# Kernel tuning notes

Measured on AMD Instinct MI355X. Metric: run time of the kernel, lower is better.

The kernel has to match this reference:

```python
import jax, jax.numpy as jnp
import numpy as np

L = 3          # num_layers
H = 128        # hidden_dim
NH = 4         # num heads
DH = H // NH   # head dim
B = 32         # graphs per batch
N = 1024       # nodes per graph
NTOT = B * N
DEG = 16
E = NTOT * DEG
BN_EPS = 1e-5


def setup_inputs() -> dict:
    key = jax.random.key(0)
    ks = jax.random.split(key, 16)
    s = 1.0 / np.sqrt(H)
    inp = {
        "x": jax.random.normal(ks[0], (NTOT, H), jnp.float32),
        "edge_attr": jax.random.normal(ks[1], (E, H), jnp.float32),
        "gine_w1": jax.random.normal(ks[2], (L, H, H), jnp.float32) * s,
        "gine_b1": jnp.zeros((L, H), jnp.float32),
        "gine_bn_g": jnp.ones((L, H), jnp.float32),
        "gine_bn_b": jnp.zeros((L, H), jnp.float32),
        "gine_w2": jax.random.normal(ks[3], (L, H, H), jnp.float32) * s,
        "gine_b2": jnp.zeros((L, H), jnp.float32),
        "attn_wqkv": jax.random.normal(ks[4], (L, 3 * H, H), jnp.float32) * s,
        "attn_bqkv": jnp.zeros((L, 3 * H), jnp.float32),
        "attn_wo": jax.random.normal(ks[5], (L, H, H), jnp.float32) * s,
        "attn_bo": jnp.zeros((L, H), jnp.float32),
        "norm1_g": jnp.ones((L, H), jnp.float32),
        "norm1_b": jnp.zeros((L, H), jnp.float32),
        "norm2_g": jnp.ones((L, H), jnp.float32),
        "norm2_b": jnp.zeros((L, H), jnp.float32),
        "norm3_g": jnp.ones((L, H), jnp.float32),
        "norm3_b": jnp.zeros((L, H), jnp.float32),
        "mlp_w1": jax.random.normal(ks[6], (L, 2 * H, H), jnp.float32) * s,
        "mlp_b1": jnp.zeros((L, 2 * H), jnp.float32),
        "mlp_w2": jax.random.normal(ks[7], (L, H, 2 * H), jnp.float32) * (1.0 / np.sqrt(2 * H)),
        "mlp_b2": jnp.zeros((L, H), jnp.float32),
    }
    # intra-graph random edges: local src/dst in [0, N) plus per-graph offset
    offs = (jnp.arange(E, dtype=jnp.int32) // (N * DEG)) * N  # graph offset per edge
    src = jax.random.randint(ks[8], (E,), 0, N, jnp.int32) + offs
    dst = jax.random.randint(ks[9], (E,), 0, N, jnp.int32) + offs
    inp["edge_index"] = jnp.stack([src, dst]).astype(jnp.int32)
    inp["batch"] = (jnp.arange(NTOT, dtype=jnp.int32) // N)
    return inp


def _bn(x, g, b):
    m = x.mean(axis=0)
    v = jnp.var(x, axis=0)
    return (x - m) * jax.lax.rsqrt(v + BN_EPS) * g + b


def _gps_forward(x, edge_attr, gine_w1, gine_b1, gine_bn_g, gine_bn_b, gine_w2, gine_b2,
                 attn_wqkv, attn_bqkv, attn_wo, attn_bo,
                 norm1_g, norm1_b, norm2_g, norm2_b, norm3_g, norm3_b,
                 mlp_w1, mlp_b1, mlp_w2, mlp_b2, edge_index, batch):
    src, dst = edge_index[0], edge_index[1]
    for i in range(L):
        # ---- GINEConv: msg = relu(x_j + e), sum-scatter, nn-MLP on x + aggr (eps=0)
        msg = jax.nn.relu(x[src] + edge_attr)                       # [E, H]
        aggr = jax.ops.segment_sum(msg, dst, num_segments=NTOT)     # [NTOT, H]
        h = x + aggr
        h = h @ gine_w1[i].T + gine_b1[i]
        h = jax.nn.relu(_bn(h, gine_bn_g[i], gine_bn_b[i]))
        h = h @ gine_w2[i].T + gine_b2[i]
        h_local = _bn(h + x, norm1_g[i], norm1_b[i])                # residual + norm1
        # ---- global multi-head attention on x (dense per-graph, equal sizes)
        xb = x.reshape(B, N, H)
        qkv = xb @ attn_wqkv[i].T + attn_bqkv[i]                    # [B, N, 3H]
        q, k, v = jnp.split(qkv, 3, axis=-1)
        q = q.reshape(B, N, NH, DH).transpose(0, 2, 1, 3)           # [B, nh, N, dh]
        k = k.reshape(B, N, NH, DH).transpose(0, 2, 1, 3)
        v = v.reshape(B, N, NH, DH).transpose(0, 2, 1, 3)
        scores = jnp.einsum("bhqd,bhkd->bhqk", q, k) / np.sqrt(DH)
        attn = jax.nn.softmax(scores, axis=-1)
        o = jnp.einsum("bhqk,bhkd->bhqd", attn, v)
        o = o.transpose(0, 2, 1, 3).reshape(B, N, H) @ attn_wo[i].T + attn_bo[i]
        h_attn = _bn(o.reshape(NTOT, H) + x, norm2_g[i], norm2_b[i])
        # ---- combine + FFN + norm3
        out = h_local + h_attn
        ff = jax.nn.relu(out @ mlp_w1[i].T + mlp_b1[i]) @ mlp_w2[i].T + mlp_b2[i]
        x = _bn(out + ff, norm3_g[i], norm3_b[i])
        if i != L - 1:
            x = jax.nn.relu(x)
    return x


def reference(x, edge_attr, gine_w1, gine_b1, gine_bn_g, gine_bn_b, gine_w2, gine_b2,
              attn_wqkv, attn_bqkv, attn_wo, attn_bo,
              norm1_g, norm1_b, norm2_g, norm2_b, norm3_g, norm3_b,
              mlp_w1, mlp_b1, mlp_w2, mlp_b2, edge_index, batch):
    return _gps_forward(x, edge_attr, gine_w1, gine_b1, gine_bn_g, gine_bn_b, gine_w2, gine_b2,
                        attn_wqkv, attn_bqkv, attn_wo, attn_bo,
                        norm1_g, norm1_b, norm2_g, norm2_b, norm3_g, norm3_b,
                        mlp_w1, mlp_b1, mlp_w2, mlp_b2, edge_index, batch)
```

## Files before the change

kernel.cpp:

```cpp
#include <hip/hip_runtime.h>
#include <hip/hip_bf16.h>
#include <math.h>

#define NTOT 32768
#define HDIM 128
#define NE   524288
#define NGRAPH 32
#define NNODE 1024
#define NHEAD 4
#define DHEAD 32

typedef __attribute__((ext_vector_type(8))) short bf8v;
typedef __attribute__((ext_vector_type(4))) float f4v;
typedef unsigned short u16;

__device__ __forceinline__ float4 ld4(const float* p){ return *(const float4*)p; }

__device__ __forceinline__ u16 bf16rn(float f){
  union { float f; unsigned u; } x; x.f = f;
  unsigned r = x.u + 0x7FFF + ((x.u >> 16) & 1);
  return (u16)(r >> 16);
}
__device__ __forceinline__ unsigned pk2(float a, float b){
  unsigned r;
  asm("v_cvt_pk_bf16_f32 %0, %1, %2" : "=v"(r) : "v"(a), "v"(b));
  return r;
}
__device__ __forceinline__ float bf2f(u16 u){
  union { unsigned u; float f; } x; x.u = ((unsigned)u) << 16;
  return x.f;
}

__global__ void k_count(const int* __restrict__ dst, int* __restrict__ deg){
  int e = blockIdx.x*256 + threadIdx.x;
  atomicAdd(&deg[dst[e]], 1);
}

__global__ __launch_bounds__(1024) void k_scan(const int* __restrict__ deg,
                                               int* __restrict__ indptr,
                                               int* __restrict__ cursor){
  __shared__ int sm[1024];
  int t = threadIdx.x;
  int base = t*32;
  int s = 0;
  for (int j=0;j<32;j++) s += deg[base+j];
  sm[t] = s; __syncthreads();
  for (int off=1; off<1024; off<<=1){
    int v = (t>=off) ? sm[t-off] : 0;
    __syncthreads();
    sm[t] += v;
    __syncthreads();
  }
  int ex = sm[t] - s;
  for (int j=0;j<32;j++){
    int d = deg[base+j];
    indptr[base+j] = ex; cursor[base+j] = ex;
    ex += d;
  }
  if (t == 1023) indptr[NTOT] = ex;
}

__global__ void k_fill(const int* __restrict__ dst, int* __restrict__ cursor,
                       int* __restrict__ perm){
  int e = blockIdx.x*256 + threadIdx.x;
  int pos = atomicAdd(&cursor[dst[e]], 1);
  perm[pos] = e;
}

__global__ __launch_bounds__(256) void k_eaprep(const float* __restrict__ ea,
    const int* __restrict__ src, const int* __restrict__ perm,
    u16* __restrict__ EAb, int* __restrict__ SRCp){
  int tid = threadIdx.x;
  int p = blockIdx.x*8 + (tid>>5);
  int c4 = (tid&31)*4;
  int e = perm[p];
  float4 v = ld4(&ea[(size_t)e*HDIM + c4]);
  uint2 o; o.x = pk2(v.x, v.y); o.y = pk2(v.z, v.w);
  *(uint2*)&EAb[(size_t)p*HDIM + c4] = o;
  if ((tid&31) == 0) SRCp[p] = src[e];
}

__global__ __launch_bounds__(256) void k_xprep(const float* __restrict__ x, u16* __restrict__ Xb){
  size_t i = ((size_t)blockIdx.x*256 + threadIdx.x)*4;
  float4 v = ld4(&x[i]);
  uint2 o; o.x = pk2(v.x,v.y); o.y = pk2(v.z,v.w);
  *(uint2*)&Xb[i] = o;
}

__global__ __launch_bounds__(256) void k_wprep(const float* s0,const float* s1,const float* s2,
    const float* s3,const float* s4,const float* s5, u16* __restrict__ Wb){
  const float* srcs[6] = {s0,s1,s2,s3,s4,s5};
  const int cnt4[6] = {12288,12288,36864,12288,24576,24576};
  const int off[6]  = {0,49152,98304,245760,294912,393216};
  int y = blockIdx.y;
  int i = blockIdx.x*256 + threadIdx.x;
  if (i >= cnt4[y]) return;
  float4 v = ld4(&srcs[y][(size_t)i*4]);
  uint2 o; o.x = pk2(v.x,v.y); o.y = pk2(v.z,v.w);
  *(uint2*)&Wb[off[y] + (size_t)i*4] = o;
}

__global__ __launch_bounds__(256) void k_aggr(const u16* __restrict__ Xb,
                       const u16* __restrict__ EAb,
                       const int* __restrict__ SRCp, const int* __restrict__ indptr,
                       u16* __restrict__ Hb){
  int tid = threadIdx.x;
  int n = blockIdx.x*8 + (tid>>5);
  int c4 = (tid&31)*4;
  int p0 = indptr[n], p1 = indptr[n+1];
  float a0=0.f,a1=0.f,a2=0.f,a3=0.f;
  for (int p=p0;p<p1;p++){
    int s = SRCp[p];
    uint2 xv = *(const uint2*)&Xb[(size_t)s*HDIM + c4];
    uint2 ev = *(const uint2*)&EAb[(size_t)p*HDIM + c4];
    a0 += fmaxf(bf2f((u16)(xv.x&0xffff)) + bf2f((u16)(ev.x&0xffff)), 0.f);
    a1 += fmaxf(bf2f((u16)(xv.x>>16))    + bf2f((u16)(ev.x>>16)), 0.f);
    a2 += fmaxf(bf2f((u16)(xv.y&0xffff)) + bf2f((u16)(ev.y&0xffff)), 0.f);
    a3 += fmaxf(bf2f((u16)(xv.y>>16))    + bf2f((u16)(ev.y>>16)), 0.f);
  }
  uint2 xn = *(const uint2*)&Xb[(size_t)n*HDIM + c4];
  a0 += bf2f((u16)(xn.x&0xffff)); a1 += bf2f((u16)(xn.x>>16));
  a2 += bf2f((u16)(xn.y&0xffff)); a3 += bf2f((u16)(xn.y>>16));
  uint2 o; o.x = pk2(a0,a1); o.y = pk2(a2,a3);
  *(uint2*)&Hb[(size_t)n*HDIM + c4] = o;
}

template<bool BNA, bool DUAL, bool RELU, bool EP, bool STATS, bool WROUT>
__global__ __launch_bounds__(256) void k_bgemm(const u16* __restrict__ Ab,
    const u16* __restrict__ A2b,
    const float* __restrict__ slotA, const float* __restrict__ gA, const float* __restrict__ bA,
    const float* __restrict__ slotB, const float* __restrict__ gB, const float* __restrict__ bB,
    const u16* __restrict__ Wb, const float* __restrict__ bias,
    const u16* __restrict__ Epb, u16* __restrict__ Cb,
    u16* __restrict__ OUTb, float* __restrict__ slotOut, int N, int K){
  __shared__ float sbnA[256];
  __shared__ float sbnB[256];
  __shared__ float sred[128];
  int tid = threadIdx.x;
  int w = tid>>6, l = tid&63;
  int q = l&15, g = l>>4;
  int m0 = blockIdx.x*128, n0 = blockIdx.y*64;
  int wr = w*32;
  const float invn = 1.0f/32768.0f;
  if (BNA || DUAL){
    if (tid < 128){
      float mean = slotA[tid]*invn;
      float var  = slotA[128+tid]*invn - mean*mean;
      float sc = gA[tid] * rsqrtf(var + 1e-5f);
      sbnA[tid] = sc; sbnA[128+tid] = bA[tid] - mean*sc;
      if (DUAL){
        float mean2 = slotB[tid]*invn;
        float var2  = slotB[128+tid]*invn - mean2*mean2;
        float sc2 = gB[tid] * rsqrtf(var2 + 1e-5f);
        sbnB[tid] = sc2; sbnB[128+tid] = bB[tid] - mean2*sc2;
      }
    }
  }
  if (STATS && tid < 128) sred[tid] = 0.f;
  if (BNA || DUAL || STATS) __syncthreads();

  f4v acc[2][4];
  #pragma unroll
  for (int i=0;i<2;i++)
    #pragma unroll
    for (int j=0;j<4;j++) acc[i][j] = (f4v){0.f,0.f,0.f,0.f};

  for (int kc=0; kc<K; kc+=32){
    bf8v af[2], bfv[4];
    #pragma unroll
    for (int mt=0;mt<2;mt++){
      int row = m0 + wr + 16*mt + q;
      if (!BNA && !DUAL){
        af[mt] = *(const bf8v*)&Ab[(size_t)row*K + kc + 8*g];
      } else {
        union { bf8v b; u16 s[8]; unsigned u[4]; } ra, r2, ro;
        ra.b = *(const bf8v*)&Ab[(size_t)row*K + kc + 8*g];
        if (DUAL) r2.b = *(const bf8v*)&A2b[(size_t)row*K + kc + 8*g];
        float v[8];
        #pragma unroll
        for (int j=0;j<8;j++){
          int kk = kc + 8*g + j;
          float f = bf2f(ra.s[j]) * sbnA[kk] + sbnA[128+kk];
          if (BNA) f = fmaxf(f, 0.f);
          if (DUAL) f += bf2f(r2.s[j]) * sbnB[kk] + sbnB[128+kk];
          v[j] = f;
        }
        ro.u[0]=pk2(v[0],v[1]); ro.u[1]=pk2(v[2],v[3]);
        ro.u[2]=pk2(v[4],v[5]); ro.u[3]=pk2(v[6],v[7]);
        af[mt] = ro.b;
        if (WROUT && blockIdx.y == 0)
          *(uint4*)&OUTb[(size_t)row*K + kc + 8*g] = *(uint4*)ro.u;
      }
    }
    #pragma unroll
    for (int nt=0;nt<4;nt++){
      int col = n0 + 16*nt + q;
      bfv[nt] = *(const bf8v*)&Wb[(size_t)col*K + kc + 8*g];
    }
    #pragma unroll
    for (int mt=0;mt<2;mt++)
      #pragma unroll
      for (int nt=0;nt<4;nt++)
        acc[mt][nt] = __builtin_amdgcn_mfma_f32_16x16x32_bf16(af[mt], bfv[nt], acc[mt][nt], 0,0,0);
  }
  float bbv[4];
  #pragma unroll
  for (int nt=0;nt<4;nt++) bbv[nt] = bias[n0 + 16*nt + q];
  float csum[4] = {0.f,0.f,0.f,0.f}, csq[4] = {0.f,0.f,0.f,0.f};
  #pragma unroll
  for (int mt=0;mt<2;mt++){
    int row0 = m0 + wr + 16*mt + 4*g;
    #pragma unroll
    for (int nt=0;nt<4;nt++){
      int col = n0 + 16*nt + q;
      #pragma unroll
      for (int r=0;r<4;r++){
        size_t off = (size_t)(row0+r)*N + col;
        float v = acc[mt][nt][r] + bbv[nt];
        if (EP) v += bf2f(Epb[off]);
        if (RELU) v = fmaxf(v, 0.f);
        Cb[off] = bf16rn(v);
        if (STATS){ csum[nt] += v; csq[nt] += v*v; }
      }
    }
  }
  if (STATS){
    #pragma unroll
    for (int nt=0;nt<4;nt++){
      int c = 16*nt + q;
      atomicAdd(&sred[c], csum[nt]);
      atomicAdd(&sred[64+c], csq[nt]);
    }
    __syncthreads();
    if (tid < 64){
      atomicAdd(&slotOut[n0+tid], sred[tid]);
      atomicAdd(&slotOut[128+n0+tid], sred[64+tid]);
    }
  }
}

__global__ __launch_bounds__(256) void k_qkvgemm(const u16* __restrict__ Ab,
    const u16* __restrict__ Wb, const float* __restrict__ bias,
    u16* __restrict__ Qb, u16* __restrict__ Kb, u16* __restrict__ VT){
  __shared__ u16 Sm[128*72];
  int tid = threadIdx.x;
  int w = tid>>6, l = tid&63;
  int q = l&15, g = l>>4;
  int m0 = blockIdx.x*128, n0 = blockIdx.y*64;
  int which = blockIdx.y >> 1, half = blockIdx.y & 1;
  int wr = w*32;
  const int K = 128;
  f4v acc[2][4];
  #pragma unroll
  for (int i=0;i<2;i++)
    #pragma unroll
    for (int j=0;j<4;j++) acc[i][j] = (f4v){0.f,0.f,0.f,0.f};
  for (int kc=0; kc<K; kc+=32){
    bf8v af[2], bfv[4];
    #pragma unroll
    for (int mt=0;mt<2;mt++)
      af[mt] = *(const bf8v*)&Ab[(size_t)(m0+wr+16*mt+q)*K + kc + 8*g];
    #pragma unroll
    for (int nt=0;nt<4;nt++)
      bfv[nt] = *(const bf8v*)&Wb[(size_t)(n0+16*nt+q)*K + kc + 8*g];
    #pragma unroll
    for (int mt=0;mt<2;mt++)
      #pragma unroll
      for (int nt=0;nt<4;nt++)
        acc[mt][nt] = __builtin_amdgcn_mfma_f32_16x16x32_bf16(af[mt], bfv[nt], acc[mt][nt], 0,0,0);
  }
  const float QSC = 0.17677669529663687f * 1.4426950408889634f;
  float scale = (which==0) ? QSC : 1.0f;
  float bbv[4];
  #pragma unroll
  for (int nt=0;nt<4;nt++) bbv[nt] = bias[n0 + 16*nt + q];
  if (which < 2){
    #pragma unroll
    for (int mt=0;mt<2;mt++){
      int row0 = wr + 16*mt + 4*g;
      #pragma unroll
      for (int nt=0;nt<4;nt++){
        int c = 16*nt + q;
        #pragma unroll
        for (int r=0;r<4;r++)
          Sm[(row0+r)*72 + c] = bf16rn((acc[mt][nt][r] + bbv[nt]) * scale);
      }
    }
    __syncthreads();
    u16* dst = (which==0) ? Qb : Kb;
    #pragma unroll
    for (int it=0; it<4; it++){
      int idx = tid + it*256;
      int row = idx >> 3, c8 = (idx & 7) * 8;
      uint4 v = *(const uint4*)&Sm[row*72 + c8];
      *(uint4*)&dst[(size_t)(m0+row)*128 + half*64 + c8] = v;
    }
  } else {
    #pragma unroll
    for (int mt=0;mt<2;mt++){
      int row0 = wr + 16*mt + 4*g;
      #pragma unroll
      for (int nt=0;nt<4;nt++){
        int c = 16*nt + q;
        uint2 p;
        p.x = pk2(acc[mt][nt][0] + bbv[nt], acc[mt][nt][1] + bbv[nt]);
        p.y = pk2(acc[mt][nt][2] + bbv[nt], acc[mt][nt][3] + bbv[nt]);
        *(uint2*)&Sm[c*136 + row0] = p;
      }
    }
    __syncthreads();
    int gg = m0 >> 10;
    int nl0 = m0 - gg*1024;
    #pragma unroll
    for (int it=0; it<4; it++){
      int idx = tid + it*256;
      int c = idx >> 4, n8 = (idx & 15) * 8;
      uint4 v = *(const uint4*)&Sm[c*136 + n8];
      *(uint4*)&VT[((size_t)gg*128 + half*64 + c)*1024 + nl0 + n8] = v;
    }
  }
}

template<bool RELU, bool F32OUT>
__global__ __launch_bounds__(256) void k_bnapply(const u16* __restrict__ X,
    const float* __restrict__ slot, const float* __restrict__ gv, const float* __restrict__ bv,
    u16* __restrict__ Yb, float* __restrict__ Yf){
  int idx = blockIdx.x*256 + threadIdx.x;
  int row = idx >> 4, c8 = (idx & 15) * 8;
  const float invn = 1.0f/32768.0f;
  union { uint4 u; u16 s[8]; } iv;
  iv.u = *(const uint4*)&X[(size_t)row*HDIM + c8];
  float o[8];
  #pragma unroll
  for (int j=0;j<8;j++){
    int c = c8+j;
    float mean = slot[c]*invn;
    float var  = slot[128+c]*invn - mean*mean;
    float sc = gv[c] * rsqrtf(var + 1e-5f);
    float sh = bv[c] - mean*sc;
    float v = bf2f(iv.s[j])*sc + sh;
    if (RELU) v = fmaxf(v, 0.f);
    o[j] = v;
  }
  if (F32OUT){
    float* dst = &Yf[(size_t)row*HDIM + c8];
    *(float4*)dst = make_float4(o[0],o[1],o[2],o[3]);
    *(float4*)(dst+4) = make_float4(o[4],o[5],o[6],o[7]);
  } else {
    uint4 ov;
    ov.x = pk2(o[0],o[1]); ov.y = pk2(o[2],o[3]);
    ov.z = pk2(o[4],o[5]); ov.w = pk2(o[6],o[7]);
    *(uint4*)&Yb[(size_t)row*HDIM + c8] = ov;
  }
}

__global__ __launch_bounds__(256) void k_flash2(const u16* __restrict__ Qb,
    const u16* __restrict__ Kb, const u16* __restrict__ VT,
    u16* __restrict__ O){
  __shared__ u16 Pl[4][16*72];
  int tid = threadIdx.x;
  int w = tid >> 6, l = tid & 63;
  int q = l & 15, grp = l >> 4;
  int qt = blockIdx.x, h = blockIdx.y, g = blockIdx.z;
  size_t gbase = (size_t)g*1024;
  size_t qrow0 = gbase + qt*64 + w*16;
  const u16* Vp = VT + ((size_t)(g*4 + h)*32)*1024;
  bf8v qf = *(const bf8v*)&Qb[(qrow0 + q)*128 + h*32 + 8*grp];
  u16* Pw = &Pl[w][0];
  float m = -1e30f, lsum = 0.f;
  f4v o0 = {0.f,0.f,0.f,0.f}, o1 = {0.f,0.f,0.f,0.f};
  for (int kt=0; kt<16; kt++){
    int k0 = kt*64;
    f4v st[4];
    #pragma unroll
    for (int t=0;t<4;t++){
      bf8v kf = *(const bf8v*)&Kb[(gbase + k0 + 16*t + q)*128 + h*32 + 8*grp];
      st[t] = __builtin_amdgcn_mfma_f32_16x16x32_bf16(kf, qf, (f4v){0.f,0.f,0.f,0.f}, 0,0,0);
    }
    float smax = st[0][0];
    #pragma unroll
    for (int t=0;t<4;t++)
      #pragma unroll
      for (int r=0;r<4;r++) smax = fmaxf(smax, st[t][r]);
    smax = fmaxf(smax, __shfl_xor(smax, 16));
    smax = fmaxf(smax, __shfl_xor(smax, 32));
    float mnew = fmaxf(m, smax);
    float alpha = exp2f(m - mnew);
    float psum = 0.f;
    #pragma unroll
    for (int t=0;t<4;t++){
      float p0 = exp2f(st[t][0]-mnew), p1 = exp2f(st[t][1]-mnew);
      float p2 = exp2f(st[t][2]-mnew), p3 = exp2f(st[t][3]-mnew);
      psum += (p0+p1)+(p2+p3);
      *(unsigned*)&Pw[q*72 + 16*t + 4*grp]     = pk2(p0,p1);
      *(unsigned*)&Pw[q*72 + 16*t + 4*grp + 2] = pk2(p2,p3);
    }
    psum += __shfl_xor(psum, 16);
    psum += __shfl_xor(psum, 32);
    lsum = lsum*alpha + psum;
    m = mnew;
    f4v aD;
    #pragma unroll
    for (int r=0;r<4;r++) aD[r] = __shfl(alpha, 4*grp + r);
    #pragma unroll
    for (int r=0;r<4;r++){ o0[r] *= aD[r]; o1[r] *= aD[r]; }
    bf8v pa0 = *(const bf8v*)&Pw[q*72 + 8*grp];
    bf8v pa1 = *(const bf8v*)&Pw[q*72 + 32 + 8*grp];
    bf8v v00 = *(const bf8v*)&Vp[(size_t)q*1024      + k0 + 8*grp];
    bf8v v01 = *(const bf8v*)&Vp[(size_t)q*1024      + k0 + 32 + 8*grp];
    bf8v v10 = *(const bf8v*)&Vp[(size_t)(16+q)*1024 + k0 + 8*grp];
    bf8v v11 = *(const bf8v*)&Vp[(size_t)(16+q)*1024 + k0 + 32 + 8*grp];
    o0 = __builtin_amdgcn_mfma_f32_16x16x32_bf16(pa0, v00, o0, 0,0,0);
    o0 = __builtin_amdgcn_mfma_f32_16x16x32_bf16(pa1, v01, o0, 0,0,0);
    o1 = __builtin_amdgcn_mfma_f32_16x16x32_bf16(pa0, v10, o1, 0,0,0);
    o1 = __builtin_amdgcn_mfma_f32_16x16x32_bf16(pa1, v11, o1, 0,0,0);
  }
  f4v lD;
  #pragma unroll
  for (int r=0;r<4;r++) lD[r] = __shfl(lsum, 4*grp + r);
  #pragma unroll
  for (int r=0;r<4;r++){
    float inv = 1.0f/lD[r];
    size_t row = qrow0 + 4*grp + r;
    O[row*HDIM + h*32 + q]      = bf16rn(o0[r]*inv);
    O[row*HDIM + h*32 + 16 + q] = bf16rn(o1[r]*inv);
  }
}

extern "C" void kernel_launch(void* const* d_in, const int* in_sizes, int n_in,
                              void* d_out, int out_size, void* d_ws, size_t ws_size,
                              hipStream_t stream){
  const float* x_in      = (const float*)d_in[0];
  const float* edge_attr = (const float*)d_in[1];
  const float* gine_w1   = (const float*)d_in[2];
  const float* gine_b1   = (const float*)d_in[3];
  const float* gine_bn_g = (const float*)d_in[4];
  const float* gine_bn_b = (const float*)d_in[5];
  const float* gine_w2   = (const float*)d_in[6];
  const float* gine_b2   = (const float*)d_in[7];
  const float* attn_wqkv = (const float*)d_in[8];
  const float* attn_bqkv = (const float*)d_in[9];
  const float* attn_wo   = (const float*)d_in[10];
  const float* attn_bo   = (const float*)d_in[11];
  const float* norm1_g   = (const float*)d_in[12];
  const float* norm1_b   = (const float*)d_in[13];
  const float* norm2_g   = (const float*)d_in[14];
  const float* norm2_b   = (const float*)d_in[15];
  const float* norm3_g   = (const float*)d_in[16];
  const float* norm3_b   = (const float*)d_in[17];
  const float* mlp_w1    = (const float*)d_in[18];
  const float* mlp_b1    = (const float*)d_in[19];
  const float* mlp_w2    = (const float*)d_in[20];
  const float* mlp_b2    = (const float*)d_in[21];
  const int* edge_index  = (const int*)d_in[22];
  const int* srcp = edge_index;
  const int* dstp = edge_index + NE;
  float* out = (float*)d_out;

  float* ws = (float*)d_ws;
  const size_t U = 4194304;
  u16* Xb   = (u16*)(ws);
  u16* Hb   = (u16*)(ws + U/2);
  u16* G1   = (u16*)(ws + U);
  u16* P1   = (u16*)(ws + U + U/2);
  u16* P2   = (u16*)(ws + 2*U);
  u16* Ob   = (u16*)(ws + 2*U + U/2);
  u16* FFb  = (u16*)(ws + 3*U);
  u16* OUTb = (u16*)(ws + 4*U);
  u16* H3   = (u16*)(ws + 4*U + U/2);
  u16* Qb   = (u16*)(ws + 5*U);
  u16* Kb   = (u16*)(ws + 5*U + U/2);
  u16* VTb  = (u16*)(ws + 6*U);
  u16* Wball= (u16*)(ws + 6*U + U/2);
  float* STATS = ws + 7*U - 8192;
  int* IW      = (int*)(ws + 7*U);
  int* deg     = IW;
  int* indptr  = IW + 32768;
  int* cursor  = IW + 32768 + 32772;
  int* perm    = cursor + 32768;
  u16* EAb  = (u16*)(ws + 8*U);
  int* SRCp = (int*)(ws + 16*U);

  u16* W1b  = Wball + 0;
  u16* W2b  = Wball + 49152;
  u16* WQb  = Wball + 98304;
  u16* WOb  = Wball + 245760;
  u16* WM1b = Wball + 294912;
  u16* WM2b = Wball + 393216;

  hipMemsetAsync(STATS, 0, 12*512*sizeof(float), stream);
  hipMemsetAsync(deg, 0, NTOT*sizeof(int), stream);
  k_count<<<NE/256, 256, 0, stream>>>(dstp, deg);
  k_scan<<<1, 1024, 0, stream>>>(deg, indptr, cursor);
  k_fill<<<NE/256, 256, 0, stream>>>(dstp, cursor, perm);
  k_eaprep<<<NE/8, 256, 0, stream>>>(edge_attr, srcp, perm, EAb, SRCp);
  k_xprep<<<4096, 256, 0, stream>>>(x_in, Xb);
  k_wprep<<<dim3(144,6), 256, 0, stream>>>(gine_w1, gine_w2, attn_wqkv, attn_wo, mlp_w1, mlp_w2, Wball);

  dim3 gN128(NTOT/128, 2), gN256(NTOT/128, 4), gQKV(NTOT/128, 6);

  for (int i=0;i<3;i++){
    const float* B1 = gine_b1 + (size_t)i*HDIM;
    const float* B2 = gine_b2 + (size_t)i*HDIM;
    const float* BQ = attn_bqkv + (size_t)i*3*HDIM;
    const float* BO = attn_bo + (size_t)i*HDIM;
    const float* BM1 = mlp_b1 + (size_t)i*2*HDIM;
    const float* BM2 = mlp_b2 + (size_t)i*HDIM;
    u16* w1 = W1b + (size_t)i*16384;
    u16* w2 = W2b + (size_t)i*16384;
    u16* wq = WQb + (size_t)i*49152;
    u16* wo = WOb + (size_t)i*16384;
    u16* wm1 = WM1b + (size_t)i*32768;
    u16* wm2 = WM2b + (size_t)i*32768;
    float* S0 = STATS + (size_t)(i*4+0)*512;
    float* S1 = STATS + (size_t)(i*4+1)*512;
    float* S2 = STATS + (size_t)(i*4+2)*512;
    float* S3 = STATS + (size_t)(i*4+3)*512;
    const float* bnG = gine_bn_g + (size_t)i*HDIM;
    const float* bnB = gine_bn_b + (size_t)i*HDIM;
    const float* n1g = norm1_g + (size_t)i*HDIM, *n1b = norm1_b + (size_t)i*HDIM;
    const float* n2g = norm2_g + (size_t)i*HDIM, *n2b = norm2_b + (size_t)i*HDIM;
    const float* n3g = norm3_g + (size_t)i*HDIM, *n3b = norm3_b + (size_t)i*HDIM;

    k_aggr<<<NTOT/8, 256, 0, stream>>>(Xb, EAb, SRCp, indptr, Hb);
    k_bgemm<false,false,false,false,true,false><<<gN128, 256, 0, stream>>>(
      Hb, nullptr, nullptr,nullptr,nullptr, nullptr,nullptr,nullptr,
      w1, B1, nullptr, G1, nullptr, S0, 128, 128);
    k_bgemm<true,false,false,true,true,false><<<gN128, 256, 0, stream>>>(
      G1, nullptr, S0, bnG, bnB, nullptr,nullptr,nullptr,
      w2, B2, Xb, P1, nullptr, S1, 128, 128);

    k_qkvgemm<<<gQKV, 256, 0, stream>>>(Xb, wq, BQ, Qb, Kb, VTb);
    k_flash2<<<dim3(16, NHEAD, NGRAPH), 256, 0, stream>>>(Qb, Kb, VTb, Ob);
    k_bgemm<false,false,false,true,true,false><<<gN128, 256, 0, stream>>>(
      Ob, nullptr, nullptr,nullptr,nullptr, nullptr,nullptr,nullptr,
      wo, BO, Xb, P2, nullptr, S2, 128, 128);

    k_bgemm<false,true,true,false,false,true><<<gN256, 256, 0, stream>>>(
      P1, P2, S1, n1g, n1b, S2, n2g, n2b,
      wm1, BM1, nullptr, FFb, OUTb, nullptr, 256, 128);
    k_bgemm<false,false,false,true,true,false><<<gN128, 256, 0, stream>>>(
      FFb, nullptr, nullptr,nullptr,nullptr, nullptr,nullptr,nullptr,
      wm2, BM2, OUTb, H3, nullptr, S3, 128, 256);

    if (i<2) k_bnapply<true ,false><<<2048, 256, 0, stream>>>(H3, S3, n3g, n3b, Xb, nullptr);
    else     k_bnapply<false,true ><<<2048, 256, 0, stream>>>(H3, S3, n3g, n3b, nullptr, out);
  }
}
```

Measured before the change: 1.049 ms.

## Fuse BN-apply into consumers, merge prep kernels, retile GEMMs to full-width rows

The per-layer norm3 BN+ReLU pass is removed. Its normalization is now applied on the fly in the next layer's aggregation, QKV GEMM and residual epilogues, with the pre-norm buffers double-buffered. The three prep kernels are merged into one launch, and the two memsets become one. GEMMs switch to 64-row tiles covering all output columns, which drops the column-split grid and duplicated A loads. The aggregation splits each node's edges across two half-waves with a prefetched source index. The BN transform is recomputed redundantly in several consumers, and the new tiles have fewer blocks and more accumulators per wave.

New measurement: 1.188 ms. 13.3% more time.

```diff
diff --git a/kernel.cpp b/kernel.cpp
--- a/kernel.cpp
+++ b/kernel.cpp
@@ -67,264 +67,302 @@
   perm[pos] = e;
 }
 
-__global__ __launch_bounds__(256) void k_eaprep(const float* __restrict__ ea,
+__global__ __launch_bounds__(256) void k_prep(const float* __restrict__ ea,
     const int* __restrict__ src, const int* __restrict__ perm,
-    u16* __restrict__ EAb, int* __restrict__ SRCp){
+    u16* __restrict__ EAb, int* __restrict__ SRCp,
+    const float* __restrict__ x, u16* __restrict__ Xb,
+    const float* s0,const float* s1,const float* s2,
+    const float* s3,const float* s4,const float* s5, u16* __restrict__ Wb){
+  int b = blockIdx.x, tid = threadIdx.x;
+  if (b < 65536){
+    int p = b*8 + (tid>>5);
+    int c4 = (tid&31)*4;
+    int e = perm[p];
+    float4 v = ld4(&ea[(size_t)e*HDIM + c4]);
+    uint2 o; o.x = pk2(v.x, v.y); o.y = pk2(v.z, v.w);
+    *(uint2*)&EAb[(size_t)p*HDIM + c4] = o;
+    if ((tid&31) == 0) SRCp[p] = src[e];
+  } else if (b < 69632){
+    size_t i = ((size_t)(b-65536)*256 + tid)*4;
+    float4 v = ld4(&x[i]);
+    uint2 o; o.x = pk2(v.x,v.y); o.y = pk2(v.z,v.w);
+    *(uint2*)&Xb[i] = o;
+  } else {
+    int idx = b - 69632;
+    int y = idx / 144;
+    int i = (idx % 144)*256 + tid;
+    const float* srcs[6] = {s0,s1,s2,s3,s4,s5};
+    const int cnt4[6] = {12288,12288,36864,12288,24576,24576};
+    const int off[6]  = {0,49152,98304,245760,294912,393216};
+    if (i < cnt4[y]){
+      float4 v = ld4(&srcs[y][(size_t)i*4]);
+      uint2 o; o.x = pk2(v.x,v.y); o.y = pk2(v.z,v.w);
+      *(uint2*)&Wb[off[y] + (size_t)i*4] = o;
+    }
+  }
+}
+
+template<bool XF>
+__global__ __launch_bounds__(256) void k_aggr(const u16* __restrict__ Xc,
+    const float* __restrict__ slotX, const float* __restrict__ gX, const float* __restrict__ bX,
+    const u16* __restrict__ EAb, const int* __restrict__ SRCp,
+    const int* __restrict__ indptr, u16* __restrict__ Hb){
   int tid = threadIdx.x;
-  int p = blockIdx.x*8 + (tid>>5);
-  int c4 = (tid&31)*4;
-  int e = perm[p];
-  float4 v = ld4(&ea[(size_t)e*HDIM + c4]);
-  uint2 o; o.x = pk2(v.x, v.y); o.y = pk2(v.z, v.w);
-  *(uint2*)&EAb[(size_t)p*HDIM + c4] = o;
-  if ((tid&31) == 0) SRCp[p] = src[e];
-}
-
-__global__ __launch_bounds__(256) void k_xprep(const float* __restrict__ x, u16* __restrict__ Xb){
-  size_t i = ((size_t)blockIdx.x*256 + threadIdx.x)*4;
-  float4 v = ld4(&x[i]);
-  uint2 o; o.x = pk2(v.x,v.y); o.y = pk2(v.z,v.w);
-  *(uint2*)&Xb[i] = o;
-}
-
-__global__ __launch_bounds__(256) void k_wprep(const float* s0,const float* s1,const float* s2,
-    const float* s3,const float* s4,const float* s5, u16* __restrict__ Wb){
-  const float* srcs[6] = {s0,s1,s2,s3,s4,s5};
-  const int cnt4[6] = {12288,12288,36864,12288,24576,24576};
-  const int off[6]  = {0,49152,98304,245760,294912,393216};
-  int y = blockIdx.y;
-  int i = blockIdx.x*256 + threadIdx.x;
-  if (i >= cnt4[y]) return;
-  float4 v = ld4(&srcs[y][(size_t)i*4]);
-  uint2 o; o.x = pk2(v.x,v.y); o.y = pk2(v.z,v.w);
-  *(uint2*)&Wb[off[y] + (size_t)i*4] = o;
-}
-
-__global__ __launch_bounds__(256) void k_aggr(const u16* __restrict__ Xb,
-                       const u16* __restrict__ EAb,
-                       const int* __restrict__ SRCp, const int* __restrict__ indptr,
-                       u16* __restrict__ Hb){
-  int tid = threadIdx.x;
-  int n = blockIdx.x*8 + (tid>>5);
-  int c4 = (tid&31)*4;
+  int w = tid>>6, lane = tid&63, half = lane>>5, cl = lane&31;
+  int c4 = cl*4;
+  int n = blockIdx.x*4 + w;
+  float sc[4], sh[4];
+  if (XF){
+    const float invn = 1.0f/32768.0f;
+    #pragma unroll
+    for (int j=0;j<4;j++){
+      int c = c4+j;
+      float mean = slotX[c]*invn;
+      float var  = slotX[128+c]*invn - mean*mean;
+      float s = gX[c] * rsqrtf(var + 1e-5f);
+      sc[j] = s; sh[j] = bX[c] - mean*s;
+    }
+  }
   int p0 = indptr[n], p1 = indptr[n+1];
   float a0=0.f,a1=0.f,a2=0.f,a3=0.f;
-  for (int p=p0;p<p1;p++){
-    int s = SRCp[p];
-    uint2 xv = *(const uint2*)&Xb[(size_t)s*HDIM + c4];
+  int p = p0 + half;
+  int sNext = (p < p1) ? SRCp[p] : 0;
+  for (; p < p1; p += 2){
+    int s = sNext;
+    if (p+2 < p1) sNext = SRCp[p+2];
     uint2 ev = *(const uint2*)&EAb[(size_t)p*HDIM + c4];
-    a0 += fmaxf(bf2f((u16)(xv.x&0xffff)) + bf2f((u16)(ev.x&0xffff)), 0.f);
-    a1 += fmaxf(bf2f((u16)(xv.x>>16))    + bf2f((u16)(ev.x>>16)), 0.f);
-    a2 += fmaxf(bf2f((u16)(xv.y&0xffff)) + bf2f((u16)(ev.y&0xffff)), 0.f);
-    a3 += fmaxf(bf2f((u16)(xv.y>>16))    + bf2f((u16)(ev.y>>16)), 0.f);
-  }
-  uint2 xn = *(const uint2*)&Xb[(size_t)n*HDIM + c4];
-  a0 += bf2f((u16)(xn.x&0xffff)); a1 += bf2f((u16)(xn.x>>16));
-  a2 += bf2f((u16)(xn.y&0xffff)); a3 += bf2f((u16)(xn.y>>16));
-  uint2 o; o.x = pk2(a0,a1); o.y = pk2(a2,a3);
-  *(uint2*)&Hb[(size_t)n*HDIM + c4] = o;
-}
-
-template<bool BNA, bool DUAL, bool RELU, bool EP, bool STATS, bool WROUT>
+    uint2 xv = *(const uint2*)&Xc[(size_t)s*HDIM + c4];
+    float x0 = bf2f((u16)(xv.x&0xffff)), x1 = bf2f((u16)(xv.x>>16));
+    float x2 = bf2f((u16)(xv.y&0xffff)), x3 = bf2f((u16)(xv.y>>16));
+    if (XF){
+      x0 = fmaxf(x0*sc[0]+sh[0], 0.f); x1 = fmaxf(x1*sc[1]+sh[1], 0.f);
+      x2 = fmaxf(x2*sc[2]+sh[2], 0.f); x3 = fmaxf(x3*sc[3]+sh[3], 0.f);
+    }
+    a0 += fmaxf(x0 + bf2f((u16)(ev.x&0xffff)), 0.f);
+    a1 += fmaxf(x1 + bf2f((u16)(ev.x>>16)), 0.f);
+    a2 += fmaxf(x2 + bf2f((u16)(ev.y&0xffff)), 0.f);
+    a3 += fmaxf(x3 + bf2f((u16)(ev.y>>16)), 0.f);
+  }
+  a0 += __shfl_xor(a0, 32); a1 += __shfl_xor(a1, 32);
+  a2 += __shfl_xor(a2, 32); a3 += __shfl_xor(a3, 32);
+  if (half == 0){
+    uint2 xn = *(const uint2*)&Xc[(size_t)n*HDIM + c4];
+    float x0 = bf2f((u16)(xn.x&0xffff)), x1 = bf2f((u16)(xn.x>>16));
+    float x2 = bf2f((u16)(xn.y&0xffff)), x3 = bf2f((u16)(xn.y>>16));
+    if (XF){
+      x0 = fmaxf(x0*sc[0]+sh[0], 0.f); x1 = fmaxf(x1*sc[1]+sh[1], 0.f);
+      x2 = fmaxf(x2*sc[2]+sh[2], 0.f); x3 = fmaxf(x3*sc[3]+sh[3], 0.f);
+    }
+    a0 += x0; a1 += x1; a2 += x2; a3 += x3;
+    uint2 o; o.x = pk2(a0,a1); o.y = pk2(a2,a3);
+    *(uint2*)&Hb[(size_t)n*HDIM + c4] = o;
+  }
+}
+
+template<int SM, int EM, bool RELU, bool STATS, bool WROUT, int NT>
 __global__ __launch_bounds__(256) void k_bgemm(const u16* __restrict__ Ab,
     const u16* __restrict__ A2b,
     const float* __restrict__ slotA, const float* __restrict__ gA, const float* __restrict__ bA,
     const float* __restrict__ slotB, const float* __restrict__ gB, const float* __restrict__ bB,
     const u16* __restrict__ Wb, const float* __restrict__ bias,
     const u16* __restrict__ Epb, u16* __restrict__ Cb,
-    u16* __restrict__ OUTb, float* __restrict__ slotOut, int N, int K){
-  __shared__ float sbnA[256];
-  __shared__ float sbnB[256];
-  __shared__ float sred[128];
+    u16* __restrict__ OUTb, float* __restrict__ slotOut, int K){
+  __shared__ float sbn1[256];
+  __shared__ float sbn2[256];
+  __shared__ float sred[256];
+  const int N = NT*16;
   int tid = threadIdx.x;
   int w = tid>>6, l = tid&63;
   int q = l&15, g = l>>4;
-  int m0 = blockIdx.x*128, n0 = blockIdx.y*64;
-  int wr = w*32;
+  int m0 = blockIdx.x*64;
   const float invn = 1.0f/32768.0f;
-  if (BNA || DUAL){
-    if (tid < 128){
-      float mean = slotA[tid]*invn;
-      float var  = slotA[128+tid]*invn - mean*mean;
-      float sc = gA[tid] * rsqrtf(var + 1e-5f);
-      sbnA[tid] = sc; sbnA[128+tid] = bA[tid] - mean*sc;
-      if (DUAL){
-        float mean2 = slotB[tid]*invn;
-        float var2  = slotB[128+tid]*invn - mean2*mean2;
-        float sc2 = gB[tid] * rsqrtf(var2 + 1e-5f);
-        sbnB[tid] = sc2; sbnB[128+tid] = bB[tid] - mean2*sc2;
+  if ((SM >= 1) && tid < 128){
+    float mean = slotA[tid]*invn;
+    float var  = slotA[128+tid]*invn - mean*mean;
+    float s = gA[tid] * rsqrtf(var + 1e-5f);
+    sbn1[tid] = s; sbn1[128+tid] = bA[tid] - mean*s;
+  }
+  if ((SM == 2 || EM == 2) && tid < 128){
+    float mean = slotB[tid]*invn;
+    float var  = slotB[128+tid]*invn - mean*mean;
+    float s = gB[tid] * rsqrtf(var + 1e-5f);
+    sbn2[tid] = s; sbn2[128+tid] = bB[tid] - mean*s;
+  }
+  if (STATS && tid < 128){ sred[tid] = 0.f; sred[128+tid] = 0.f; }
+  if (SM >= 1 || EM == 2 || STATS) __syncthreads();
+
+  f4v acc[NT];
+  #pragma unroll
+  for (int j=0;j<NT;j++) acc[j] = (f4v){0.f,0.f,0.f,0.f};
+
+  int row = m0 + w*16 + q;
+  for (int kc=0; kc<K; kc+=32){
+    bf8v af;
+    if (SM == 0){
+      af = *(const bf8v*)&Ab[(size_t)row*K + kc + 8*g];
+    } else {
+      union { bf8v b; u16 s[8]; unsigned u[4]; } ra, r2, ro;
+      ra.b = *(const bf8v*)&Ab[(size_t)row*K + kc + 8*g];
+      if (SM == 2) r2.b = *(const bf8v*)&A2b[(size_t)row*K + kc + 8*g];
+      float v[8];
+      #pragma unroll
+      for (int j=0;j<8;j++){
+        int kk = kc + 8*g + j;
+        float f = bf2f(ra.s[j]) * sbn1[kk] + sbn1[128+kk];
+        if (SM == 1) f = fmaxf(f, 0.f);
+        if (SM == 2) f += bf2f(r2.s[j]) * sbn2[kk] + sbn2[128+kk];
+        v[j] = f;
       }
-    }
-  }
-  if (STATS && tid < 128) sred[tid] = 0.f;
-  if (BNA || DUAL || STATS) __syncthreads();
-
-  f4v acc[2][4];
-  #pragma unroll
-  for (int i=0;i<2;i++)
-    #pragma unroll
-    for (int j=0;j<4;j++) acc[i][j] = (f4v){0.f,0.f,0.f,0.f};
-
-  for (int kc=0; kc<K; kc+=32){
-    bf8v af[2], bfv[4];
-    #pragma unroll
-    for (int mt=0;mt<2;mt++){
-      int row = m0 + wr + 16*mt + q;
-      if (!BNA && !DUAL){
-        af[mt] = *(const bf8v*)&Ab[(size_t)row*K + kc + 8*g];
-      } else {
-        union { bf8v b; u16 s[8]; unsigned u[4]; } ra, r2, ro;
-        ra.b = *(const bf8v*)&Ab[(size_t)row*K + kc + 8*g];
-        if (DUAL) r2.b = *(const bf8v*)&A2b[(size_t)row*K + kc + 8*g];
-        float v[8];
-        #pragma unroll
-        for (int j=0;j<8;j++){
-          int kk = kc + 8*g + j;
-          float f = bf2f(ra.s[j]) * sbnA[kk] + sbnA[128+kk];
-          if (BNA) f = fmaxf(f, 0.f);
-          if (DUAL) f += bf2f(r2.s[j]) * sbnB[kk] + sbnB[128+kk];
-          v[j] = f;
-        }
-        ro.u[0]=pk2(v[0],v[1]); ro.u[1]=pk2(v[2],v[3]);
-        ro.u[2]=pk2(v[4],v[5]); ro.u[3]=pk2(v[6],v[7]);
-        af[mt] = ro.b;
-        if (WROUT && blockIdx.y == 0)
-          *(uint4*)&OUTb[(size_t)row*K + kc + 8*g] = *(uint4*)ro.u;
+      ro.u[0]=pk2(v[0],v[1]); ro.u[1]=pk2(v[2],v[3]);
+      ro.u[2]=pk2(v[4],v[5]); ro.u[3]=pk2(v[6],v[7]);
+      af = ro.b;
+      if (WROUT) *(uint4*)&OUTb[(size_t)row*K + kc + 8*g] = *(uint4*)ro.u;
+    }
+    #pragma unroll
+    for (int nt=0;nt<NT;nt++){
+      bf8v bv = *(const bf8v*)&Wb[(size_t)(16*nt+q)*K + kc + 8*g];
+      acc[nt] = __builtin_amdgcn_mfma_f32_16x16x32_bf16(af, bv, acc[nt], 0,0,0);
+    }
+  }
+  float bbv[NT];
+  #pragma unroll
+  for (int nt=0;nt<NT;nt++) bbv[nt] = bias[16*nt + q];
+  int row0 = m0 + w*16 + 4*g;
+  float csum[STATS?NT:1], csq[STATS?NT:1];
+  if (STATS){
+    #pragma unroll
+    for (int nt=0;nt<NT;nt++){ csum[nt]=0.f; csq[nt]=0.f; }
+  }
+  #pragma unroll
+  for (int nt=0;nt<NT;nt++){
+    int col = 16*nt + q;
+    #pragma unroll
+    for (int r=0;r<4;r++){
+      size_t off = (size_t)(row0+r)*N + col;
+      float v = acc[nt][r] + bbv[nt];
+      if (EM == 1) v += bf2f(Epb[off]);
+      if (EM == 2){
+        float e = bf2f(Epb[off]);
+        v += fmaxf(e*sbn2[col] + sbn2[128+col], 0.f);
       }
-    }
-    #pragma unroll
-    for (int nt=0;nt<4;nt++){
-      int col = n0 + 16*nt + q;
-      bfv[nt] = *(const bf8v*)&Wb[(size_t)col*K + kc + 8*g];
-    }
-    #pragma unroll
-    for (int mt=0;mt<2;mt++)
-      #pragma unroll
-      for (int nt=0;nt<4;nt++)
-        acc[mt][nt] = __builtin_amdgcn_mfma_f32_16x16x32_bf16(af[mt], bfv[nt], acc[mt][nt], 0,0,0);
-  }
-  float bbv[4];
-  #pragma unroll
-  for (int nt=0;nt<4;nt++) bbv[nt] = bias[n0 + 16*nt + q];
-  float csum[4] = {0.f,0.f,0.f,0.f}, csq[4] = {0.f,0.f,0.f,0.f};
-  #pragma unroll
-  for (int mt=0;mt<2;mt++){
-    int row0 = m0 + wr + 16*mt + 4*g;
-    #pragma unroll
-    for (int nt=0;nt<4;nt++){
-      int col = n0 + 16*nt + q;
-      #pragma unroll
-      for (int r=0;r<4;r++){
-        size_t off = (size_t)(row0+r)*N + col;
-        float v = acc[mt][nt][r] + bbv[nt];
-        if (EP) v += bf2f(Epb[off]);
-        if (RELU) v = fmaxf(v, 0.f);
-        Cb[off] = bf16rn(v);
-        if (STATS){ csum[nt] += v; csq[nt] += v*v; }
-      }
+      if (RELU) v = fmaxf(v, 0.f);
+      Cb[off] = bf16rn(v);
+      if (STATS){ csum[nt] += v; csq[nt] += v*v; }
     }
   }
   if (STATS){
     #pragma unroll
-    for (int nt=0;nt<4;nt++){
+    for (int nt=0;nt<NT;nt++){
       int c = 16*nt + q;
       atomicAdd(&sred[c], csum[nt]);
-      atomicAdd(&sred[64+c], csq[nt]);
+      atomicAdd(&sred[128+c], csq[nt]);
     }
     __syncthreads();
-    if (tid < 64){
-      atomicAdd(&slotOut[n0+tid], sred[tid]);
-      atomicAdd(&slotOut[128+n0+tid], sred[64+tid]);
-    }
-  }
-}
-
+    if (tid < 128){
+      atomicAdd(&slotOut[tid], sred[tid]);
+      atomicAdd(&slotOut[128+tid], sred[128+tid]);
+    }
+  }
+}
+
+template<bool XF>
 __global__ __launch_bounds__(256) void k_qkvgemm(const u16* __restrict__ Ab,
+    const float* __restrict__ slotX, const float* __restrict__ gX, const float* __restrict__ bX,
     const u16* __restrict__ Wb, const float* __restrict__ bias,
     u16* __restrict__ Qb, u16* __restrict__ Kb, u16* __restrict__ VT){
-  __shared__ u16 Sm[128*72];
+  __shared__ u16 Sm[128*80];
+  __shared__ float sbn[256];
   int tid = threadIdx.x;
   int w = tid>>6, l = tid&63;
   int q = l&15, g = l>>4;
-  int m0 = blockIdx.x*128, n0 = blockIdx.y*64;
-  int which = blockIdx.y >> 1, half = blockIdx.y & 1;
-  int wr = w*32;
+  int which = blockIdx.y;
+  int m0 = blockIdx.x*64, n0 = which*128;
   const int K = 128;
-  f4v acc[2][4];
-  #pragma unroll
-  for (int i=0;i<2;i++)
-    #pragma unroll
-    for (int j=0;j<4;j++) acc[i][j] = (f4v){0.f,0.f,0.f,0.f};
+  const float invn = 1.0f/32768.0f;
+  if (XF && tid < 128){
+    float mean = slotX[tid]*invn;
+    float var  = slotX[128+tid]*invn - mean*mean;
+    float s = gX[tid] * rsqrtf(var + 1e-5f);
+    sbn[tid] = s; sbn[128+tid] = bX[tid] - mean*s;
+  }
+  if (XF) __syncthreads();
+  f4v acc[8];
+  #pragma unroll
+  for (int j=0;j<8;j++) acc[j] = (f4v){0.f,0.f,0.f,0.f};
+  int row = m0 + w*16 + q;
   for (int kc=0; kc<K; kc+=32){
-    bf8v af[2], bfv[4];
-    #pragma unroll
-    for (int mt=0;mt<2;mt++)
-      af[mt] = *(const bf8v*)&Ab[(size_t)(m0+wr+16*mt+q)*K + kc + 8*g];
-    #pragma unroll
-    for (int nt=0;nt<4;nt++)
-      bfv[nt] = *(const bf8v*)&Wb[(size_t)(n0+16*nt+q)*K + kc + 8*g];
-    #pragma unroll
-    for (int mt=0;mt<2;mt++)
+    bf8v af;
+    if (!XF){
+      af = *(const bf8v*)&Ab[(size_t)row*K + kc + 8*g];
+    } else {
+      union { bf8v b; u16 s[8]; unsigned u[4]; } ra, ro;
+      ra.b = *(const bf8v*)&Ab[(size_t)row*K + kc + 8*g];
+      float v[8];
       #pragma unroll
-      for (int nt=0;nt<4;nt++)
-        acc[mt][nt] = __builtin_amdgcn_mfma_f32_16x16x32_bf16(af[mt], bfv[nt], acc[mt][nt], 0,0,0);
+      for (int j=0;j<8;j++){
+        int kk = kc + 8*g + j;
+        v[j] = fmaxf(bf2f(ra.s[j]) * sbn[kk] + sbn[128+kk], 0.f);
+      }
+      ro.u[0]=pk2(v[0],v[1]); ro.u[1]=pk2(v[2],v[3]);
+      ro.u[2]=pk2(v[4],v[5]); ro.u[3]=pk2(v[6],v[7]);
+      af = ro.b;
+    }
+    #pragma unroll
+    for (int nt=0;nt<8;nt++){
+      bf8v bv = *(const bf8v*)&Wb[(size_t)(n0+16*nt+q)*K + kc + 8*g];
+      acc[nt] = __builtin_amdgcn_mfma_f32_16x16x32_bf16(af, bv, acc[nt], 0,0,0);
+    }
   }
   const float QSC = 0.17677669529663687f * 1.4426950408889634f;
   float scale = (which==0) ? QSC : 1.0f;
-  float bbv[4];
-  #pragma unroll
-  for (int nt=0;nt<4;nt++) bbv[nt] = bias[n0 + 16*nt + q];
+  float bbv[8];
+  #pragma unroll
+  for (int nt=0;nt<8;nt++) bbv[nt] = bias[n0 + 16*nt + q];
+  int row0 = w*16 + 4*g;
   if (which < 2){
     #pragma unroll
-    for (int mt=0;mt<2;mt++){
-      int row0 = wr + 16*mt + 4*g;
+    for (int nt=0;nt<8;nt++){
+      int c = 16*nt + q;
       #pragma unroll
-      for (int nt=0;nt<4;nt++){
-        int c = 16*nt + q;
-        #pragma unroll
-        for (int r=0;r<4;r++)
-          Sm[(row0+r)*72 + c] = bf16rn((acc[mt][nt][r] + bbv[nt]) * scale);
-      }
+      for (int r=0;r<4;r++)
+        Sm[(row0+r)*136 + c] = bf16rn((acc[nt][r] + bbv[nt]) * scale);
     }
     __syncthreads();
     u16* dst = (which==0) ? Qb : Kb;
     #pragma unroll
+    for (int it=0; it<2; it++){
+      int idx = tid + it*256;
+      int rr = idx >> 3, c8 = (idx & 7) * 16;
+      uint4 v0 = *(const uint4*)&Sm[rr*136 + c8];
+      uint4 v1 = *(const uint4*)&Sm[rr*136 + c8 + 8];
+      *(uint4*)&dst[(size_t)(m0+rr)*128 + c8] = v0;
+      *(uint4*)&dst[(size_t)(m0+rr)*128 + c8 + 8] = v1;
+    }
+  } else {
+    #pragma unroll
+    for (int nt=0;nt<8;nt++){
+      int c = 16*nt + q;
+      uint2 p;
+      p.x = pk2(acc[nt][0] + bbv[nt], acc[nt][1] + bbv[nt]);
+      p.y = pk2(acc[nt][2] + bbv[nt], acc[nt][3] + bbv[nt]);
+      *(uint2*)&Sm[c*80 + row0] = p;
+    }
+    __syncthreads();
+    int gg = m0 >> 10;
+    int nl0 = m0 & 1023;
+    #pragma unroll
     for (int it=0; it<4; it++){
       int idx = tid + it*256;
-      int row = idx >> 3, c8 = (idx & 7) * 8;
-      uint4 v = *(const uint4*)&Sm[row*72 + c8];
-      *(uint4*)&dst[(size_t)(m0+row)*128 + half*64 + c8] = v;
-    }
-  } else {
-    #pragma unroll
-    for (int mt=0;mt<2;mt++){
-      int row0 = wr + 16*mt + 4*g;
-      #pragma unroll
-      for (int nt=0;nt<4;nt++){
-        int c = 16*nt + q;
-        uint2 p;
-        p.x = pk2(acc[mt][nt][0] + bbv[nt], acc[mt][nt][1] + bbv[nt]);
-        p.y = pk2(acc[mt][nt][2] + bbv[nt], acc[mt][nt][3] + bbv[nt]);
-        *(uint2*)&Sm[c*136 + row0] = p;
-      }
-    }
-    __syncthreads();
-    int gg = m0 >> 10;
-    int nl0 = m0 - gg*1024;
-    #pragma unroll
-    for (int it=0; it<4; it++){
-      int idx = tid + it*256;
-      int c = idx >> 4, n8 = (idx & 15) * 8;
-      uint4 v = *(const uint4*)&Sm[c*136 + n8];
-      *(uint4*)&VT[((size_t)gg*128 + half*64 + c)*1024 + nl0 + n8] = v;
-    }
-  }
-}
-
-template<bool RELU, bool F32OUT>
-__global__ __launch_bounds__(256) void k_bnapply(const u16* __restrict__ X,
+      int c = idx >> 3, n8 = (idx & 7) * 8;
+      uint4 v = *(const uint4*)&Sm[c*80 + n8];
+      *(uint4*)&VT[((size_t)gg*128 + c)*1024 + nl0 + n8] = v;
+    }
+  }
+}
+
+__global__ __launch_bounds__(256) void k_bnout(const u16* __restrict__ X,
     const float* __restrict__ slot, const float* __restrict__ gv, const float* __restrict__ bv,
-    u16* __restrict__ Yb, float* __restrict__ Yf){
+    float* __restrict__ Yf){
   int idx = blockIdx.x*256 + threadIdx.x;
   int row = idx >> 4, c8 = (idx & 15) * 8;
   const float invn = 1.0f/32768.0f;
@@ -336,22 +374,12 @@
     int c = c8+j;
     float mean = slot[c]*invn;
     float var  = slot[128+c]*invn - mean*mean;
-    float sc = gv[c] * rsqrtf(var + 1e-5f);
-    float sh = bv[c] - mean*sc;
-    float v = bf2f(iv.s[j])*sc + sh;
-    if (RELU) v = fmaxf(v, 0.f);
-    o[j] = v;
-  }
-  if (F32OUT){
-    float* dst = &Yf[(size_t)row*HDIM + c8];
-    *(float4*)dst = make_float4(o[0],o[1],o[2],o[3]);
-    *(float4*)(dst+4) = make_float4(o[4],o[5],o[6],o[7]);
-  } else {
-    uint4 ov;
-    ov.x = pk2(o[0],o[1]); ov.y = pk2(o[2],o[3]);
-    ov.z = pk2(o[4],o[5]); ov.w = pk2(o[6],o[7]);
-    *(uint4*)&Yb[(size_t)row*HDIM + c8] = ov;
-  }
+    float s = gv[c] * rsqrtf(var + 1e-5f);
+    o[j] = bf2f(iv.s[j])*s + (bv[c] - mean*s);
+  }
+  float* dst = &Yf[(size_t)row*HDIM + c8];
+  *(float4*)dst = make_float4(o[0],o[1],o[2],o[3]);
+  *(float4*)(dst+4) = make_float4(o[4],o[5],o[6],o[7]);
 }
 
 __global__ __launch_bounds__(256) void k_flash2(const u16* __restrict__ Qb,
@@ -460,20 +488,21 @@
   float* ws = (float*)d_ws;
   const size_t U = 4194304;
   u16* Xb   = (u16*)(ws);
-  u16* Hb   = (u16*)(ws + U/2);
-  u16* G1   = (u16*)(ws + U);
-  u16* P1   = (u16*)(ws + U + U/2);
-  u16* P2   = (u16*)(ws + 2*U);
-  u16* Ob   = (u16*)(ws + 2*U + U/2);
-  u16* FFb  = (u16*)(ws + 3*U);
+  u16* H3a  = (u16*)(ws + U/2);
+  u16* H3b  = (u16*)(ws + U);
+  u16* Hb   = (u16*)(ws + U + U/2);
+  u16* G1   = (u16*)(ws + 2*U);
+  u16* P1   = (u16*)(ws + 2*U + U/2);
+  u16* P2   = (u16*)(ws + 3*U);
+  u16* Ob   = (u16*)(ws + 3*U + U/2);
   u16* OUTb = (u16*)(ws + 4*U);
-  u16* H3   = (u16*)(ws + 4*U + U/2);
-  u16* Qb   = (u16*)(ws + 5*U);
-  u16* Kb   = (u16*)(ws + 5*U + U/2);
-  u16* VTb  = (u16*)(ws + 6*U);
-  u16* Wball= (u16*)(ws + 6*U + U/2);
-  float* STATS = ws + 7*U - 8192;
-  int* IW      = (int*)(ws + 7*U);
+  u16* FFb  = (u16*)(ws + 4*U + U/2);
+  u16* Qb   = (u16*)(ws + 5*U + U/2);
+  u16* Kb   = (u16*)(ws + 6*U);
+  u16* VTb  = (u16*)(ws + 6*U + U/2);
+  u16* Wball= (u16*)(ws + 7*U);
+  float* STATS = ws + 7*U + U/4;
+  int* IW      = (int*)(STATS + 12*512);
   int* deg     = IW;
   int* indptr  = IW + 32768;
   int* cursor  = IW + 32768 + 32772;
@@ -488,16 +517,15 @@
   u16* WM1b = Wball + 294912;
   u16* WM2b = Wball + 393216;
 
-  hipMemsetAsync(STATS, 0, 12*512*sizeof(float), stream);
-  hipMemsetAsync(deg, 0, NTOT*sizeof(int), stream);
+  hipMemsetAsync(STATS, 0, (12*512)*sizeof(float) + NTOT*sizeof(int), stream);
   k_count<<<NE/256, 256, 0, stream>>>(dstp, deg);
   k_scan<<<1, 1024, 0, stream>>>(deg, indptr, cursor);
   k_fill<<<NE/256, 256, 0, stream>>>(dstp, cursor, perm);
-  k_eaprep<<<NE/8, 256, 0, stream>>>(edge_attr, srcp, perm, EAb, SRCp);
-  k_xprep<<<4096, 256, 0, stream>>>(x_in, Xb);
-  k_wprep<<<dim3(144,6), 256, 0, stream>>>(gine_w1, gine_w2, attn_wqkv, attn_wo, mlp_w1, mlp_w2, Wball);
-
-  dim3 gN128(NTOT/128, 2), gN256(NTOT/128, 4), gQKV(NTOT/128, 6);
+  k_prep<<<70496, 256, 0, stream>>>(edge_attr, srcp, perm, EAb, SRCp, x_in, Xb,
+                                    gine_w1, gine_w2, attn_wqkv, attn_wo, mlp_w1, mlp_w2, Wball);
+
+  const u16* NUL16 = nullptr;
+  const float* NULF = nullptr;
 
   for (int i=0;i<3;i++){
     const float* B1 = gine_b1 + (size_t)i*HDIM;
@@ -522,28 +550,39 @@
     const float* n2g = norm2_g + (size_t)i*HDIM, *n2b = norm2_b + (size_t)i*HDIM;
     const float* n3g = norm3_g + (size_t)i*HDIM, *n3b = norm3_b + (size_t)i*HDIM;
 
-    k_aggr<<<NTOT/8, 256, 0, stream>>>(Xb, EAb, SRCp, indptr, Hb);
-    k_bgemm<false,false,false,false,true,false><<<gN128, 256, 0, stream>>>(
-      Hb, nullptr, nullptr,nullptr,nullptr, nullptr,nullptr,nullptr,
-      w1, B1, nullptr, G1, nullptr, S0, 128, 128);
-    k_bgemm<true,false,false,true,true,false><<<gN128, 256, 0, stream>>>(
-      G1, nullptr, S0, bnG, bnB, nullptr,nullptr,nullptr,
-      w2, B2, Xb, P1, nullptr, S1, 128, 128);
-
-    k_qkvgemm<<<gQKV, 256, 0, stream>>>(Xb, wq, BQ, Qb, Kb, VTb);
+    const u16* Xc = (i==0) ? Xb : (i==1 ? H3a : H3b);
+    u16* H3 = (i==0) ? H3a : (i==1 ? H3b : H3a);
+    float* SX = (i==0) ? nullptr : STATS + (size_t)((i-1)*4+3)*512;
+    const float* gx = (i==0) ? nullptr : norm3_g + (size_t)(i-1)*HDIM;
+    const float* bx = (i==0) ? nullptr : norm3_b + (size_t)(i-1)*HDIM;
+
+    if (i==0) k_aggr<false><<<NTOT/4, 256, 0, stream>>>(Xc, NULF,NULF,NULF, EAb, SRCp, indptr, Hb);
+    else      k_aggr<true ><<<NTOT/4, 256, 0, stream>>>(Xc, SX, gx, bx, EAb, SRCp, indptr, Hb);
+    k_bgemm<0,0,false,true,false,8><<<512, 256, 0, stream>>>(
+      Hb, NUL16, NULF,NULF,NULF, NULF,NULF,NULF, w1, B1, NUL16, G1, nullptr, S0, 128);
+    if (i==0)
+      k_bgemm<1,1,false,true,false,8><<<512, 256, 0, stream>>>(
+        G1, NUL16, S0, bnG, bnB, NULF,NULF,NULF, w2, B2, Xc, P1, nullptr, S1, 128);
+    else
+      k_bgemm<1,2,false,true,false,8><<<512, 256, 0, stream>>>(
+        G1, NUL16, S0, bnG, bnB, SX, gx, bx, w2, B2, Xc, P1, nullptr, S1, 128);
+
+    if (i==0) k_qkvgemm<false><<<dim3(512,3), 256, 0, stream>>>(Xc, NULF,NULF,NULF, wq, BQ, Qb, Kb, VTb);
+    else      k_qkvgemm<true ><<<dim3(512,3), 256, 0, stream>>>(Xc, SX, gx, bx, wq, BQ, Qb, Kb, VTb);
     k_flash2<<<dim3(16, NHEAD, NGRAPH), 256, 0, stream>>>(Qb, Kb, VTb, Ob);
-    k_bgemm<false,false,false,true,true,false><<<gN128, 256, 0, stream>>>(
-      Ob, nullptr, nullptr,nullptr,nullptr, nullptr,nullptr,nullptr,
-      wo, BO, Xb, P2, nullptr, S2, 128, 128);
-
-    k_bgemm<false,true,true,false,false,true><<<gN256, 256, 0, stream>>>(
-      P1, P2, S1, n1g, n1b, S2, n2g, n2b,
-      wm1, BM1, nullptr, FFb, OUTb, nullptr, 256, 128);
-    k_bgemm<false,false,false,true,true,false><<<gN128, 256, 0, stream>>>(
-      FFb, nullptr, nullptr,nullptr,nullptr, nullptr,nullptr,nullptr,
-      wm2, BM2, OUTb, H3, nullptr, S3, 128, 256);
-
-    if (i<2) k_bnapply<true ,false><<<2048, 256, 0, stream>>>(H3, S3, n3g, n3b, Xb, nullptr);
-    else     k_bnapply<false,true ><<<2048, 256, 0, stream>>>(H3, S3, n3g, n3b, nullptr, out);
-  }
-}
+    if (i==0)
+      k_bgemm<0,1,false,true,false,8><<<512, 256, 0, stream>>>(
+        Ob, NUL16, NULF,NULF,NULF, NULF,NULF,NULF, wo, BO, Xc, P2, nullptr, S2, 128);
+    else
+      k_bgemm<0,2,false,true,false,8><<<512, 256, 0, stream>>>(
+        Ob, NUL16, NULF,NULF,NULF, SX, gx, bx, wo, BO, Xc, P2, nullptr, S2, 128);
+
+    k_bgemm<2,0,true,false,true,16><<<512, 256, 0, stream>>>(
+      P1, P2, S1, n1g, n1b, S2, n2g, n2b, wm1, BM1, NUL16, FFb, OUTb, nullptr, 128);
+    k_bgemm<0,1,false,true,false,8><<<512, 256, 0, stream>>>(
+      FFb, NUL16, NULF,NULF,NULF, NULF,NULF,NULF, wm2, BM2, OUTb, H3, nullptr, S3, 256);
+
+    if (i==2)
+      k_bnout<<<2048, 256, 0, stream>>>(H3, S3, n3g, n3b, out);
+  }
+}
```
